# Performance work log

Measured on AMD Instinct MI355X. Metric: run time of the kernel, lower is better.

Reference implementation:

```python
import math
import jax, jax.numpy as jnp
import numpy as np


def setup_inputs() -> dict:
    key = jax.random.key(0)
    k1, k2, k3 = jax.random.split(key, 3)
    mk = jax.random.normal(k1, (4, 64, 8, 32, 32), dtype=jnp.float32)
    qk = jax.random.normal(k2, (4, 64, 32, 32), dtype=jnp.float32)
    mv = jax.random.normal(k3, (4, 512, 8, 32, 32), dtype=jnp.float32)
    return {"mk": mk, "qk": qk, "mv": mv}


def reference(mk, qk, mv):
    B, CK, T, H, W = mk.shape
    CV = mv.shape[1]
    mkf = mk.reshape(B, CK, T * H * W)          # [B, CK, N]  (memory tokens)
    qkf = qk.reshape(B, CK, H * W)              # [B, CK, M]  (query tokens)
    # L2-distance style affinity: (2*a.b - |a|^2) / sqrt(CK)
    a_sq = jnp.sum(mkf * mkf, axis=1)[:, :, None]              # [B, N, 1]
    ab = jnp.einsum('bcn,bcm->bnm', mkf, qkf)                  # [B, N, M]
    affinity = (2.0 * ab - a_sq) / math.sqrt(CK)
    affinity = jax.nn.softmax(affinity, axis=1)                # softmax over memory dim
    # readout: weighted sum of memory values
    mo = mv.reshape(B, CV, T * H * W)                          # [B, CV, N]
    mem = jnp.einsum('bcn,bnm->bcm', mo, affinity)             # [B, CV, M]
    return mem.reshape(B, CV, H, W)
```

## Files before the change

kernel.cpp:

```cpp
#include <hip/hip_runtime.h>


typedef unsigned short ushort_t;
typedef unsigned int uint_t;
typedef __attribute__((ext_vector_type(8))) short short8;
typedef __attribute__((ext_vector_type(4))) float floatx4;

#define MFMA16(a, b, c) __builtin_amdgcn_mfma_f32_16x16x32_bf16((a), (b), (c), 0, 0, 0)

#define BARRIER_DS() do {                                          \
    asm volatile("s_waitcnt lgkmcnt(0)" ::: "memory");             \
    __builtin_amdgcn_s_barrier();                                  \
} while (0)

__device__ __forceinline__ ushort_t f2b(float f) {
    uint_t b = __float_as_uint(f);
    b += 0x7FFFu + ((b >> 16) & 1u);
    return (ushort_t)(b >> 16);
}

__device__ __forceinline__ short8 pack8(floatx4 a, floatx4 b) {
    short8 r;
    r[0] = (short)f2b(a[0]); r[1] = (short)f2b(a[1]);
    r[2] = (short)f2b(a[2]); r[3] = (short)f2b(a[3]);
    r[4] = (short)f2b(b[0]); r[5] = (short)f2b(b[1]);
    r[6] = (short)f2b(b[2]); r[7] = (short)f2b(b[3]);
    return r;
}

#define BB 4
#define CK 64
#define NN 8192
#define MM 1024
#define CV 512
#define NSTEP 128

__device__ __align__(16) ushort_t g_mkT[BB * NN * CK];
__device__ __align__(16) float    g_asq8[BB * NN];

__global__ __launch_bounds__(256) void k_prep(const float* __restrict__ mk) {
    int t = blockIdx.x * 256 + threadIdx.x;
    int b = t >> 13;
    int n = t & (NN - 1);
    const float* src = mk + (size_t)b * CK * NN + n;
    ushort_t* dst = g_mkT + (size_t)t * CK;
    float acc = 0.f;
#pragma unroll
    for (int g = 0; g < 8; g++) {
        float f[8];
#pragma unroll
        for (int i = 0; i < 8; i++) {
            f[i] = src[(size_t)(g * 8 + i) * NN];
            acc += f[i] * f[i];
        }
        uint4 q;
        q.x = (uint_t)f2b(f[0]) | ((uint_t)f2b(f[1]) << 16);
        q.y = (uint_t)f2b(f[2]) | ((uint_t)f2b(f[3]) << 16);
        q.z = (uint_t)f2b(f[4]) | ((uint_t)f2b(f[5]) << 16);
        q.w = (uint_t)f2b(f[6]) | ((uint_t)f2b(f[7]) << 16);
        *(uint4*)(dst + g * 8) = q;
    }
    g_asq8[t] = acc * 0.125f;
}


#define STEP(KC0, KC1, AC, MC0, MC1, MC2, MC3, KN0, KN1, AN, MN0, MN1, MN2, MN3, stepv) do { \
    if ((stepv) + 1 < NSTEP) {                                                  \
        size_t no = (size_t)((stepv) + 1) * 64;                                 \
        const ushort_t* kp = kbase + no * CK;                                   \
        KN0 = *(const short8*)kp;                                               \
        KN1 = *(const short8*)(kp + 32);                                        \
        AN  = asbase[no];                                                       \
        MN0 = *(const floatx4*)(mvbase + no);                                   \
        MN1 = *(const floatx4*)(mvbase + no + 4);                               \
        MN2 = *(const floatx4*)(mvbase + no + 32);                              \
        MN3 = *(const floatx4*)(mvbase + no + 36);                              \
    }                                                                           \
    _Pragma("unroll")                                                           \
    for (int mt = 0; mt < 4; mt++) {                                            \
        floatx4 d = (floatx4){0.f, 0.f, 0.f, 0.f};                              \
        d = MFMA16(qb0[mt], KC0, d);                                            \
        d = MFMA16(qb1[mt], KC1, d);                                            \
        _Pragma("unroll")                                                       \
        for (int r = 0; r < 4; r++) {                                           \
            float p = __expf(d[r] * 0.25f - AC);                                \
            dpart[mt][r] += p;                                                  \
            lds_p[(mt * 16 + quad * 4 + r) * 72 + w * 16 + l15] = f2b(p);       \
        }                                                                       \
    }                                                                           \
    BARRIER_DS();        \
    {                                                                           \
        short8 va0 = pack8(MC0, MC1);                                           \
        short8 va1 = pack8(MC2, MC3);                                           \
        _Pragma("unroll")                                                       \
        for (int mt = 0; mt < 4; mt++) {                                        \
            short8 pb0 = *(const short8*)&lds_p[(mt * 16 + l15) * 72 + quad * 8];        \
            short8 pb1 = *(const short8*)&lds_p[(mt * 16 + l15) * 72 + 32 + quad * 8];   \
            acc[mt] = MFMA16(va0, pb0, acc[mt]);                                \
            acc[mt] = MFMA16(va1, pb1, acc[mt]);                                \
        }                                                                       \
    }                                                                           \
    BARRIER_DS();                         \
} while (0)

__global__ __launch_bounds__(256, 2) void k_main(const float* __restrict__ qk,
                                                 const float* __restrict__ mv,
                                                 float* __restrict__ out) {
    __shared__ __align__(16) ushort_t lds_p[64 * 72];
    __shared__ float dn[64];

    int bx = blockIdx.x;
    int mt16 = bx >> 5;
    int cs = (bx >> 2) & 7;
    int b = bx & 3;
    int c0 = cs * 64;
    int m0 = mt16 * 64;

    int tid = threadIdx.x;
    int w = tid >> 6;
    int lane = tid & 63;
    int quad = lane >> 4;
    int l15 = lane & 15;

    if (tid < 64) dn[tid] = 0.f;

    short8 qb0[4], qb1[4];
#pragma unroll
    for (int mt = 0; mt < 4; mt++) {
#pragma unroll
        for (int j = 0; j < 8; j++) {
            qb0[mt][j] = (short)f2b(qk[(size_t)(b * CK + quad * 8 + j) * MM + m0 + mt * 16 + l15]);
            qb1[mt][j] = (short)f2b(qk[(size_t)(b * CK + 32 + quad * 8 + j) * MM + m0 + mt * 16 + l15]);
        }
    }

    const ushort_t* kbase  = g_mkT + ((size_t)b * NN + w * 16 + l15) * CK + quad * 8;
    const float*    asbase = g_asq8 + (size_t)b * NN + w * 16 + l15;
    const float*    mvbase = mv + ((size_t)(b * CV + c0 + w * 16 + l15)) * NN + quad * 8;

    floatx4 acc[4];
#pragma unroll
    for (int i = 0; i < 4; i++) acc[i] = (floatx4){0.f, 0.f, 0.f, 0.f};
    float dpart[4][4];
#pragma unroll
    for (int i = 0; i < 4; i++)
#pragma unroll
        for (int j = 0; j < 4; j++) dpart[i][j] = 0.f;

    short8 kA0, kA1, kB0, kB1;
    floatx4 mA0, mA1, mA2, mA3, mB0, mB1, mB2, mB3;
    float aA, aB;
    kA0 = *(const short8*)kbase;
    kA1 = *(const short8*)(kbase + 32);
    aA  = *asbase;
    mA0 = *(const floatx4*)(mvbase);
    mA1 = *(const floatx4*)(mvbase + 4);
    mA2 = *(const floatx4*)(mvbase + 32);
    mA3 = *(const floatx4*)(mvbase + 36);

    for (int sp = 0; sp < NSTEP / 2; sp++) {
        STEP(kA0, kA1, aA, mA0, mA1, mA2, mA3, kB0, kB1, aB, mB0, mB1, mB2, mB3, sp * 2);
        STEP(kB0, kB1, aB, mB0, mB1, mB2, mB3, kA0, kA1, aA, mA0, mA1, mA2, mA3, sp * 2 + 1);
    }

#pragma unroll
    for (int mt = 0; mt < 4; mt++) {
#pragma unroll
        for (int r = 0; r < 4; r++) {
            float s = dpart[mt][r];
            s += __shfl_xor(s, 1, 64);
            s += __shfl_xor(s, 2, 64);
            s += __shfl_xor(s, 4, 64);
            s += __shfl_xor(s, 8, 64);
            if (l15 == 0) atomicAdd(&dn[mt * 16 + quad * 4 + r], s);
        }
    }
    __syncthreads();

    float rdm[4];
#pragma unroll
    for (int mt = 0; mt < 4; mt++) rdm[mt] = 1.0f / dn[mt * 16 + l15];
#pragma unroll
    for (int mt = 0; mt < 4; mt++) {
#pragma unroll
        for (int r = 0; r < 4; r++) {
            size_t o = (size_t)(b * CV + c0 + w * 16 + quad * 4 + r) * MM
                     + m0 + mt * 16 + l15;
            out[o] = acc[mt][r] * rdm[mt];
        }
    }
}

extern "C" void kernel_launch(void* const* d_in, const int* in_sizes, int n_in,
                              void* d_out, int out_size, void* d_ws, size_t ws_size,
                              hipStream_t stream) {
    const float* mk = nullptr;
    const float* qk = nullptr;
    const float* mv = nullptr;
    for (int i = 0; i < n_in; i++) {
        if (in_sizes[i] == BB * CK * NN)      mk = (const float*)d_in[i];
        else if (in_sizes[i] == BB * CK * MM) qk = (const float*)d_in[i];
        else if (in_sizes[i] == BB * CV * NN) mv = (const float*)d_in[i];
    }
    float* out = (float*)d_out;
    (void)d_ws; (void)ws_size; (void)out_size;

    k_prep<<<(BB * NN) / 256, 256, 0, stream>>>(mk);
    k_main<<<16 * 8 * BB, 256, 0, stream>>>(qk, mv, out);
}
```

Baseline: 270.4 us.

## Split memory dimension across two blocks with reduction kernel; coalesce prep transpose

Splits the N (memory token) loop into two halves handled by separate blocks, doubling the grid from 512 to 1024 blocks and raising occupancy hints. Partial numerators and denominators go to global scratch and a new reduce kernel combines and normalizes them. The prep kernel is rewritten to transpose mk through LDS with vectorized coalesced loads. The split adds an extra kernel launch, a partial-result round trip through global memory, and reloads qk once per half. The softmax stays correct because the exponentials carry no max subtraction.

```diff
diff --git a/kernel.cpp b/kernel.cpp
--- a/kernel.cpp
+++ b/kernel.cpp
@@ -33,39 +33,59 @@
 #define NN 8192
 #define MM 1024
 #define CV 512
-#define NSTEP 128
+#define NH 2
+#define NSTEP_H 64
 
 __device__ __align__(16) ushort_t g_mkT[BB * NN * CK];
 __device__ __align__(16) float    g_asq8[BB * NN];
+__device__ __align__(16) float    g_pacc[1024 * 64 * 64];
+__device__ __align__(16) float    g_pdn[1024 * 64];
 
 __global__ __launch_bounds__(256) void k_prep(const float* __restrict__ mk) {
-    int t = blockIdx.x * 256 + threadIdx.x;
-    int b = t >> 13;
-    int n = t & (NN - 1);
-    const float* src = mk + (size_t)b * CK * NN + n;
-    ushort_t* dst = g_mkT + (size_t)t * CK;
-    float acc = 0.f;
-#pragma unroll
-    for (int g = 0; g < 8; g++) {
-        float f[8];
-#pragma unroll
-        for (int i = 0; i < 8; i++) {
-            f[i] = src[(size_t)(g * 8 + i) * NN];
-            acc += f[i] * f[i];
-        }
-        uint4 q;
-        q.x = (uint_t)f2b(f[0]) | ((uint_t)f2b(f[1]) << 16);
-        q.y = (uint_t)f2b(f[2]) | ((uint_t)f2b(f[3]) << 16);
-        q.z = (uint_t)f2b(f[4]) | ((uint_t)f2b(f[5]) << 16);
-        q.w = (uint_t)f2b(f[6]) | ((uint_t)f2b(f[7]) << 16);
-        *(uint4*)(dst + g * 8) = q;
-    }
-    g_asq8[t] = acc * 0.125f;
+    __shared__ float lds_t[64][68];
+    int bx = blockIdx.x;
+    int b = bx >> 7;
+    int nt = bx & 127;
+    int tid = threadIdx.x;
+    int cc = tid >> 2, seg = tid & 3;
+    const float* src = mk + ((size_t)(b * CK + cc)) * NN + nt * 64 + seg * 16;
+#pragma unroll
+    for (int g = 0; g < 4; g++) {
+        floatx4 v = *(const floatx4*)(src + g * 4);
+        lds_t[seg * 16 + g * 4 + 0][cc] = v[0];
+        lds_t[seg * 16 + g * 4 + 1][cc] = v[1];
+        lds_t[seg * 16 + g * 4 + 2][cc] = v[2];
+        lds_t[seg * 16 + g * 4 + 3][cc] = v[3];
+    }
+    __syncthreads();
+    int n = tid >> 2;
+    const float* row = &lds_t[n][seg * 16];
+    float v[16];
+#pragma unroll
+    for (int i = 0; i < 16; i++) v[i] = row[i];
+    float sq = 0.f;
+#pragma unroll
+    for (int i = 0; i < 16; i++) sq = fmaf(v[i], v[i], sq);
+    sq += __shfl_xor(sq, 1, 64);
+    sq += __shfl_xor(sq, 2, 64);
+    uint4 q0, q1;
+    q0.x = (uint_t)f2b(v[0])  | ((uint_t)f2b(v[1])  << 16);
+    q0.y = (uint_t)f2b(v[2])  | ((uint_t)f2b(v[3])  << 16);
+    q0.z = (uint_t)f2b(v[4])  | ((uint_t)f2b(v[5])  << 16);
+    q0.w = (uint_t)f2b(v[6])  | ((uint_t)f2b(v[7])  << 16);
+    q1.x = (uint_t)f2b(v[8])  | ((uint_t)f2b(v[9])  << 16);
+    q1.y = (uint_t)f2b(v[10]) | ((uint_t)f2b(v[11]) << 16);
+    q1.z = (uint_t)f2b(v[12]) | ((uint_t)f2b(v[13]) << 16);
+    q1.w = (uint_t)f2b(v[14]) | ((uint_t)f2b(v[15]) << 16);
+    ushort_t* dst = g_mkT + ((size_t)b * NN + nt * 64 + n) * CK + seg * 16;
+    *(uint4*)dst = q0;
+    *(uint4*)(dst + 8) = q1;
+    if (seg == 0) g_asq8[(size_t)b * NN + nt * 64 + n] = sq * 0.125f;
 }
 
 
 #define STEP(KC0, KC1, AC, MC0, MC1, MC2, MC3, KN0, KN1, AN, MN0, MN1, MN2, MN3, stepv) do { \
-    if ((stepv) + 1 < NSTEP) {                                                  \
+    if ((stepv) + 1 < NSTEP_H) {                                                \
         size_t no = (size_t)((stepv) + 1) * 64;                                 \
         const ushort_t* kp = kbase + no * CK;                                   \
         KN0 = *(const short8*)kp;                                               \
@@ -103,18 +123,19 @@
     BARRIER_DS();                         \
 } while (0)
 
-__global__ __launch_bounds__(256, 2) void k_main(const float* __restrict__ qk,
-                                                 const float* __restrict__ mv,
-                                                 float* __restrict__ out) {
+__global__ __launch_bounds__(256, 4) void k_main(const float* __restrict__ qk,
+                                                 const float* __restrict__ mv) {
     __shared__ __align__(16) ushort_t lds_p[64 * 72];
     __shared__ float dn[64];
 
     int bx = blockIdx.x;
-    int mt16 = bx >> 5;
-    int cs = (bx >> 2) & 7;
-    int b = bx & 3;
+    int mt16 = bx >> 6;
+    int cs = (bx >> 3) & 7;
+    int b = (bx >> 1) & 3;
+    int nh = bx & 1;
     int c0 = cs * 64;
     int m0 = mt16 * 64;
+    int n0 = nh * (NN / NH);
 
     int tid = threadIdx.x;
     int w = tid >> 6;
@@ -134,9 +155,9 @@
         }
     }
 
-    const ushort_t* kbase  = g_mkT + ((size_t)b * NN + w * 16 + l15) * CK + quad * 8;
-    const float*    asbase = g_asq8 + (size_t)b * NN + w * 16 + l15;
-    const float*    mvbase = mv + ((size_t)(b * CV + c0 + w * 16 + l15)) * NN + quad * 8;
+    const ushort_t* kbase  = g_mkT + ((size_t)b * NN + n0 + w * 16 + l15) * CK + quad * 8;
+    const float*    asbase = g_asq8 + (size_t)b * NN + n0 + w * 16 + l15;
+    const float*    mvbase = mv + ((size_t)(b * CV + c0 + w * 16 + l15)) * NN + n0 + quad * 8;
 
     floatx4 acc[4];
 #pragma unroll
@@ -158,7 +179,7 @@
     mA2 = *(const floatx4*)(mvbase + 32);
     mA3 = *(const floatx4*)(mvbase + 36);
 
-    for (int sp = 0; sp < NSTEP / 2; sp++) {
+    for (int sp = 0; sp < NSTEP_H / 2; sp++) {
         STEP(kA0, kA1, aA, mA0, mA1, mA2, mA3, kB0, kB1, aB, mB0, mB1, mB2, mB3, sp * 2);
         STEP(kB0, kB1, aB, mB0, mB1, mB2, mB3, kA0, kA1, aA, mA0, mA1, mA2, mA3, sp * 2 + 1);
     }
@@ -177,17 +198,43 @@
     }
     __syncthreads();
 
-    float rdm[4];
-#pragma unroll
-    for (int mt = 0; mt < 4; mt++) rdm[mt] = 1.0f / dn[mt * 16 + l15];
+    float* pa = g_pacc + (size_t)bx * 4096;
 #pragma unroll
     for (int mt = 0; mt < 4; mt++) {
 #pragma unroll
-        for (int r = 0; r < 4; r++) {
-            size_t o = (size_t)(b * CV + c0 + w * 16 + quad * 4 + r) * MM
-                     + m0 + mt * 16 + l15;
-            out[o] = acc[mt][r] * rdm[mt];
-        }
+        for (int r = 0; r < 4; r++)
+            pa[(w * 16 + quad * 4 + r) * 64 + mt * 16 + l15] = acc[mt][r];
+    }
+    if (tid < 64) g_pdn[(size_t)bx * 64 + tid] = dn[tid];
+}
+
+__global__ __launch_bounds__(256) void k_reduce(float* __restrict__ out) {
+    __shared__ float rdm[64];
+    int bxr = blockIdx.x;
+    int mt16 = bxr >> 5;
+    int cs = (bxr >> 2) & 7;
+    int b = bxr & 3;
+    int tid = threadIdx.x;
+
+    const float* p0 = g_pacc + (size_t)(2 * bxr) * 4096;
+    const float* p1 = g_pacc + (size_t)(2 * bxr + 1) * 4096;
+    if (tid < 64)
+        rdm[tid] = 1.0f / (g_pdn[(size_t)(2 * bxr) * 64 + tid] +
+                           g_pdn[(size_t)(2 * bxr + 1) * 64 + tid]);
+    __syncthreads();
+
+    int c_loc = tid >> 2;
+    int mseg = (tid & 3) * 16;
+    size_t pbase = (size_t)c_loc * 64 + mseg;
+    size_t obase = (size_t)(b * CV + cs * 64 + c_loc) * MM + mt16 * 64 + mseg;
+#pragma unroll
+    for (int g4 = 0; g4 < 4; g4++) {
+        floatx4 a = *(const floatx4*)(p0 + pbase + g4 * 4);
+        floatx4 bb = *(const floatx4*)(p1 + pbase + g4 * 4);
+        floatx4 r;
+#pragma unroll
+        for (int j = 0; j < 4; j++) r[j] = (a[j] + bb[j]) * rdm[mseg + g4 * 4 + j];
+        *(floatx4*)(out + obase + g4 * 4) = r;
     }
 }
 
@@ -205,6 +252,7 @@
     float* out = (float*)d_out;
     (void)d_ws; (void)ws_size; (void)out_size;
 
-    k_prep<<<(BB * NN) / 256, 256, 0, stream>>>(mk);
-    k_main<<<16 * 8 * BB, 256, 0, stream>>>(qk, mv, out);
-}
+    k_prep<<<BB * 128, 256, 0, stream>>>(mk);
+    k_main<<<16 * 8 * BB * NH, 256, 0, stream>>>(qk, mv);
+    k_reduce<<<16 * 8 * BB, 256, 0, stream>>>(out);
+}
```

New measurement: 372.7 us. 37.8% more time.

## Split main kernel into producer/consumer waves with double-buffered P tile

Applied to the files above, without the earlier changes.

The main kernel moves to 512 threads. Four producer waves compute the affinity exponentials into one of two LDS buffers while four consumer waves load mv and run the readout MFMAs on the other buffer, so the exp/softmax stage and the value GEMM overlap across steps. The prep kernel now transposes mk through LDS with coalesced vector loads instead of strided scalar reads. The trade-offs are more threads per block, doubled LDS, and producers and consumers staying in lockstep through barriers.

```diff
diff --git a/kernel.cpp b/kernel.cpp
--- a/kernel.cpp
+++ b/kernel.cpp
@@ -39,43 +39,64 @@
 __device__ __align__(16) float    g_asq8[BB * NN];
 
 __global__ __launch_bounds__(256) void k_prep(const float* __restrict__ mk) {
-    int t = blockIdx.x * 256 + threadIdx.x;
-    int b = t >> 13;
-    int n = t & (NN - 1);
-    const float* src = mk + (size_t)b * CK * NN + n;
-    ushort_t* dst = g_mkT + (size_t)t * CK;
-    float acc = 0.f;
-#pragma unroll
-    for (int g = 0; g < 8; g++) {
-        float f[8];
-#pragma unroll
-        for (int i = 0; i < 8; i++) {
-            f[i] = src[(size_t)(g * 8 + i) * NN];
-            acc += f[i] * f[i];
-        }
-        uint4 q;
-        q.x = (uint_t)f2b(f[0]) | ((uint_t)f2b(f[1]) << 16);
-        q.y = (uint_t)f2b(f[2]) | ((uint_t)f2b(f[3]) << 16);
-        q.z = (uint_t)f2b(f[4]) | ((uint_t)f2b(f[5]) << 16);
-        q.w = (uint_t)f2b(f[6]) | ((uint_t)f2b(f[7]) << 16);
-        *(uint4*)(dst + g * 8) = q;
-    }
-    g_asq8[t] = acc * 0.125f;
-}
-
-
-#define STEP(KC0, KC1, AC, MC0, MC1, MC2, MC3, KN0, KN1, AN, MN0, MN1, MN2, MN3, stepv) do { \
-    if ((stepv) + 1 < NSTEP) {                                                  \
-        size_t no = (size_t)((stepv) + 1) * 64;                                 \
-        const ushort_t* kp = kbase + no * CK;                                   \
-        KN0 = *(const short8*)kp;                                               \
-        KN1 = *(const short8*)(kp + 32);                                        \
-        AN  = asbase[no];                                                       \
-        MN0 = *(const floatx4*)(mvbase + no);                                   \
-        MN1 = *(const floatx4*)(mvbase + no + 4);                               \
-        MN2 = *(const floatx4*)(mvbase + no + 32);                              \
-        MN3 = *(const floatx4*)(mvbase + no + 36);                              \
-    }                                                                           \
+    __shared__ float lds_t[64][68];
+    int bx = blockIdx.x;
+    int b = bx >> 7;
+    int nt = bx & 127;
+    int tid = threadIdx.x;
+    int cc = tid >> 2, seg = tid & 3;
+    const float* src = mk + ((size_t)(b * CK + cc)) * NN + nt * 64 + seg * 16;
+#pragma unroll
+    for (int g = 0; g < 4; g++) {
+        floatx4 v = *(const floatx4*)(src + g * 4);
+        lds_t[seg * 16 + g * 4 + 0][cc] = v[0];
+        lds_t[seg * 16 + g * 4 + 1][cc] = v[1];
+        lds_t[seg * 16 + g * 4 + 2][cc] = v[2];
+        lds_t[seg * 16 + g * 4 + 3][cc] = v[3];
+    }
+    __syncthreads();
+    int n = tid >> 2;
+    const float* row = &lds_t[n][seg * 16];
+    float v[16];
+#pragma unroll
+    for (int i = 0; i < 16; i++) v[i] = row[i];
+    float sq = 0.f;
+#pragma unroll
+    for (int i = 0; i < 16; i++) sq = fmaf(v[i], v[i], sq);
+    sq += __shfl_xor(sq, 1, 64);
+    sq += __shfl_xor(sq, 2, 64);
+    uint4 q0, q1;
+    q0.x = (uint_t)f2b(v[0])  | ((uint_t)f2b(v[1])  << 16);
+    q0.y = (uint_t)f2b(v[2])  | ((uint_t)f2b(v[3])  << 16);
+    q0.z = (uint_t)f2b(v[4])  | ((uint_t)f2b(v[5])  << 16);
+    q0.w = (uint_t)f2b(v[6])  | ((uint_t)f2b(v[7])  << 16);
+    q1.x = (uint_t)f2b(v[8])  | ((uint_t)f2b(v[9])  << 16);
+    q1.y = (uint_t)f2b(v[10]) | ((uint_t)f2b(v[11]) << 16);
+    q1.z = (uint_t)f2b(v[12]) | ((uint_t)f2b(v[13]) << 16);
+    q1.w = (uint_t)f2b(v[14]) | ((uint_t)f2b(v[15]) << 16);
+    ushort_t* dst = g_mkT + ((size_t)b * NN + nt * 64 + n) * CK + seg * 16;
+    *(uint4*)dst = q0;
+    *(uint4*)(dst + 8) = q1;
+    if (seg == 0) g_asq8[(size_t)b * NN + nt * 64 + n] = sq * 0.125f;
+}
+
+
+#define PFK(KD0, KD1, AD, sv) do {                                              \
+    const ushort_t* kp = kbase + (size_t)(sv) * 64 * CK;                        \
+    KD0 = *(const short8*)kp;                                                   \
+    KD1 = *(const short8*)(kp + 32);                                            \
+    AD  = asbase[(size_t)(sv) * 64];                                            \
+} while (0)
+
+#define PFM(MD0, MD1, MD2, MD3, sv) do {                                        \
+    const float* mp = mvbase + (size_t)(sv) * 64;                               \
+    MD0 = *(const floatx4*)(mp);                                                \
+    MD1 = *(const floatx4*)(mp + 4);                                            \
+    MD2 = *(const floatx4*)(mp + 32);                                           \
+    MD3 = *(const floatx4*)(mp + 36);                                           \
+} while (0)
+
+#define PSTEP(KC0, KC1, AC, BUFID) do {                                         \
     _Pragma("unroll")                                                           \
     for (int mt = 0; mt < 4; mt++) {                                            \
         floatx4 d = (floatx4){0.f, 0.f, 0.f, 0.f};                              \
@@ -85,28 +106,27 @@
         for (int r = 0; r < 4; r++) {                                           \
             float p = __expf(d[r] * 0.25f - AC);                                \
             dpart[mt][r] += p;                                                  \
-            lds_p[(mt * 16 + quad * 4 + r) * 72 + w * 16 + l15] = f2b(p);       \
+            lds_p[BUFID][(mt * 16 + quad * 4 + r) * 72 + w * 16 + l15] = f2b(p); \
         }                                                                       \
     }                                                                           \
-    BARRIER_DS();        \
-    {                                                                           \
-        short8 va0 = pack8(MC0, MC1);                                           \
-        short8 va1 = pack8(MC2, MC3);                                           \
-        _Pragma("unroll")                                                       \
-        for (int mt = 0; mt < 4; mt++) {                                        \
-            short8 pb0 = *(const short8*)&lds_p[(mt * 16 + l15) * 72 + quad * 8];        \
-            short8 pb1 = *(const short8*)&lds_p[(mt * 16 + l15) * 72 + 32 + quad * 8];   \
-            acc[mt] = MFMA16(va0, pb0, acc[mt]);                                \
-            acc[mt] = MFMA16(va1, pb1, acc[mt]);                                \
-        }                                                                       \
+} while (0)
+
+#define CSTEP(M0, M1, M2, M3, BUFID) do {                                       \
+    short8 va0 = pack8(M0, M1);                                                 \
+    short8 va1 = pack8(M2, M3);                                                 \
+    _Pragma("unroll")                                                           \
+    for (int mt = 0; mt < 4; mt++) {                                            \
+        short8 pb0 = *(const short8*)&lds_p[BUFID][(mt * 16 + l15) * 72 + quad * 8];      \
+        short8 pb1 = *(const short8*)&lds_p[BUFID][(mt * 16 + l15) * 72 + 32 + quad * 8]; \
+        acc[mt] = MFMA16(va0, pb0, acc[mt]);                                    \
+        acc[mt] = MFMA16(va1, pb1, acc[mt]);                                    \
     }                                                                           \
-    BARRIER_DS();                         \
-} while (0)
-
-__global__ __launch_bounds__(256, 2) void k_main(const float* __restrict__ qk,
+} while (0)
+
+__global__ __launch_bounds__(512, 4) void k_main(const float* __restrict__ qk,
                                                  const float* __restrict__ mv,
                                                  float* __restrict__ out) {
-    __shared__ __align__(16) ushort_t lds_p[64 * 72];
+    __shared__ __align__(16) ushort_t lds_p[2][64 * 72];
     __shared__ float dn[64];
 
     int bx = blockIdx.x;
@@ -117,7 +137,9 @@
     int m0 = mt16 * 64;
 
     int tid = threadIdx.x;
-    int w = tid >> 6;
+    int wid = tid >> 6;
+    int w = wid & 3;
+    bool prod = wid < 4;
     int lane = tid & 63;
     int quad = lane >> 4;
     int l15 = lane & 15;
@@ -125,68 +147,84 @@
     if (tid < 64) dn[tid] = 0.f;
 
     short8 qb0[4], qb1[4];
-#pragma unroll
-    for (int mt = 0; mt < 4; mt++) {
-#pragma unroll
-        for (int j = 0; j < 8; j++) {
-            qb0[mt][j] = (short)f2b(qk[(size_t)(b * CK + quad * 8 + j) * MM + m0 + mt * 16 + l15]);
-            qb1[mt][j] = (short)f2b(qk[(size_t)(b * CK + 32 + quad * 8 + j) * MM + m0 + mt * 16 + l15]);
-        }
-    }
+    short8 kA0, kA1, kB0, kB1;
+    float aA, aB;
+    float dpart[4][4];
+    floatx4 mA0, mA1, mA2, mA3, mB0, mB1, mB2, mB3;
+    floatx4 acc[4];
 
     const ushort_t* kbase  = g_mkT + ((size_t)b * NN + w * 16 + l15) * CK + quad * 8;
     const float*    asbase = g_asq8 + (size_t)b * NN + w * 16 + l15;
     const float*    mvbase = mv + ((size_t)(b * CV + c0 + w * 16 + l15)) * NN + quad * 8;
 
-    floatx4 acc[4];
-#pragma unroll
-    for (int i = 0; i < 4; i++) acc[i] = (floatx4){0.f, 0.f, 0.f, 0.f};
-    float dpart[4][4];
-#pragma unroll
-    for (int i = 0; i < 4; i++)
-#pragma unroll
-        for (int j = 0; j < 4; j++) dpart[i][j] = 0.f;
-
-    short8 kA0, kA1, kB0, kB1;
-    floatx4 mA0, mA1, mA2, mA3, mB0, mB1, mB2, mB3;
-    float aA, aB;
-    kA0 = *(const short8*)kbase;
-    kA1 = *(const short8*)(kbase + 32);
-    aA  = *asbase;
-    mA0 = *(const floatx4*)(mvbase);
-    mA1 = *(const floatx4*)(mvbase + 4);
-    mA2 = *(const floatx4*)(mvbase + 32);
-    mA3 = *(const floatx4*)(mvbase + 36);
+    if (prod) {
+#pragma unroll
+        for (int mt = 0; mt < 4; mt++) {
+#pragma unroll
+            for (int j = 0; j < 8; j++) {
+                qb0[mt][j] = (short)f2b(qk[(size_t)(b * CK + quad * 8 + j) * MM + m0 + mt * 16 + l15]);
+                qb1[mt][j] = (short)f2b(qk[(size_t)(b * CK + 32 + quad * 8 + j) * MM + m0 + mt * 16 + l15]);
+            }
+        }
+#pragma unroll
+        for (int i = 0; i < 4; i++)
+#pragma unroll
+            for (int j = 0; j < 4; j++) dpart[i][j] = 0.f;
+        PFK(kA0, kA1, aA, 0);
+    } else {
+#pragma unroll
+        for (int i = 0; i < 4; i++) acc[i] = (floatx4){0.f, 0.f, 0.f, 0.f};
+    }
 
     for (int sp = 0; sp < NSTEP / 2; sp++) {
-        STEP(kA0, kA1, aA, mA0, mA1, mA2, mA3, kB0, kB1, aB, mB0, mB1, mB2, mB3, sp * 2);
-        STEP(kB0, kB1, aB, mB0, mB1, mB2, mB3, kA0, kA1, aA, mA0, mA1, mA2, mA3, sp * 2 + 1);
-    }
-
-#pragma unroll
-    for (int mt = 0; mt < 4; mt++) {
-#pragma unroll
-        for (int r = 0; r < 4; r++) {
-            float s = dpart[mt][r];
-            s += __shfl_xor(s, 1, 64);
-            s += __shfl_xor(s, 2, 64);
-            s += __shfl_xor(s, 4, 64);
-            s += __shfl_xor(s, 8, 64);
-            if (l15 == 0) atomicAdd(&dn[mt * 16 + quad * 4 + r], s);
-        }
+        if (prod) {
+            PFK(kB0, kB1, aB, sp * 2 + 1);
+            PSTEP(kA0, kA1, aA, 0);
+        } else {
+            PFM(mA0, mA1, mA2, mA3, sp * 2);
+            if (sp > 0) CSTEP(mB0, mB1, mB2, mB3, 1);
+        }
+        BARRIER_DS();
+        if (prod) {
+            if (sp + 1 < NSTEP / 2) PFK(kA0, kA1, aA, sp * 2 + 2);
+            PSTEP(kB0, kB1, aB, 1);
+        } else {
+            PFM(mB0, mB1, mB2, mB3, sp * 2 + 1);
+            CSTEP(mA0, mA1, mA2, mA3, 0);
+        }
+        BARRIER_DS();
+    }
+
+    if (prod) {
+#pragma unroll
+        for (int mt = 0; mt < 4; mt++) {
+#pragma unroll
+            for (int r = 0; r < 4; r++) {
+                float s = dpart[mt][r];
+                s += __shfl_xor(s, 1, 64);
+                s += __shfl_xor(s, 2, 64);
+                s += __shfl_xor(s, 4, 64);
+                s += __shfl_xor(s, 8, 64);
+                if (l15 == 0) atomicAdd(&dn[mt * 16 + quad * 4 + r], s);
+            }
+        }
+    } else {
+        CSTEP(mB0, mB1, mB2, mB3, 1);
     }
     __syncthreads();
 
-    float rdm[4];
-#pragma unroll
-    for (int mt = 0; mt < 4; mt++) rdm[mt] = 1.0f / dn[mt * 16 + l15];
-#pragma unroll
-    for (int mt = 0; mt < 4; mt++) {
-#pragma unroll
-        for (int r = 0; r < 4; r++) {
-            size_t o = (size_t)(b * CV + c0 + w * 16 + quad * 4 + r) * MM
-                     + m0 + mt * 16 + l15;
-            out[o] = acc[mt][r] * rdm[mt];
+    if (!prod) {
+        float rdm[4];
+#pragma unroll
+        for (int mt = 0; mt < 4; mt++) rdm[mt] = 1.0f / dn[mt * 16 + l15];
+#pragma unroll
+        for (int mt = 0; mt < 4; mt++) {
+#pragma unroll
+            for (int r = 0; r < 4; r++) {
+                size_t o = (size_t)(b * CV + c0 + w * 16 + quad * 4 + r) * MM
+                         + m0 + mt * 16 + l15;
+                out[o] = acc[mt][r] * rdm[mt];
+            }
         }
     }
 }
@@ -205,6 +243,6 @@
     float* out = (float*)d_out;
     (void)d_ws; (void)ws_size; (void)out_size;
 
-    k_prep<<<(BB * NN) / 256, 256, 0, stream>>>(mk);
-    k_main<<<16 * 8 * BB, 256, 0, stream>>>(qk, mv, out);
-}
+    k_prep<<<BB * 128, 256, 0, stream>>>(mk);
+    k_main<<<16 * 8 * BB, 512, 0, stream>>>(qk, mv, out);
+}
```

Result: slower. 380.5 us (+40.7%).

## Fuse key prep into main kernel, loading fp32 keys and computing norms inline

Applied to the files above, without the earlier changes.

Removes the separate prep kernel that transposed mk to bf16 and precomputed squared norms. The main kernel now reads fp32 keys directly with strided column loads, computes the per-token squared norm with cross-lane shuffles, and converts to bf16 in registers each step. This drops a kernel launch and the intermediate global round-trip. In exchange, each of the 8 channel-slice blocks per batch reloads and reconverts the keys, and each step issues 16 scalar strided loads, which adds redundant traffic and register pressure.

```diff
diff --git a/kernel.cpp b/kernel.cpp
--- a/kernel.cpp
+++ b/kernel.cpp
@@ -35,52 +35,42 @@
 #define CV 512
 #define NSTEP 128
 
-__device__ __align__(16) ushort_t g_mkT[BB * NN * CK];
-__device__ __align__(16) float    g_asq8[BB * NN];
 
-__global__ __launch_bounds__(256) void k_prep(const float* __restrict__ mk) {
-    int t = blockIdx.x * 256 + threadIdx.x;
-    int b = t >> 13;
-    int n = t & (NN - 1);
-    const float* src = mk + (size_t)b * CK * NN + n;
-    ushort_t* dst = g_mkT + (size_t)t * CK;
-    float acc = 0.f;
-#pragma unroll
-    for (int g = 0; g < 8; g++) {
-        float f[8];
-#pragma unroll
-        for (int i = 0; i < 8; i++) {
-            f[i] = src[(size_t)(g * 8 + i) * NN];
-            acc += f[i] * f[i];
-        }
-        uint4 q;
-        q.x = (uint_t)f2b(f[0]) | ((uint_t)f2b(f[1]) << 16);
-        q.y = (uint_t)f2b(f[2]) | ((uint_t)f2b(f[3]) << 16);
-        q.z = (uint_t)f2b(f[4]) | ((uint_t)f2b(f[5]) << 16);
-        q.w = (uint_t)f2b(f[6]) | ((uint_t)f2b(f[7]) << 16);
-        *(uint4*)(dst + g * 8) = q;
-    }
-    g_asq8[t] = acc * 0.125f;
-}
+#define PF(FN, MN0, MN1, MN2, MN3, sv) do {                                     \
+    size_t no = (size_t)(sv) * 64;                                              \
+    _Pragma("unroll")                                                           \
+    for (int j = 0; j < 8; j++) {                                               \
+        FN[j]     = kb[(size_t)j * NN + no];                                    \
+        FN[j + 8] = kb[(size_t)(32 + j) * NN + no];                             \
+    }                                                                           \
+    const float* mp = mvbase + no;                                              \
+    MN0 = *(const floatx4*)(mp);                                                \
+    MN1 = *(const floatx4*)(mp + 4);                                            \
+    MN2 = *(const floatx4*)(mp + 32);                                           \
+    MN3 = *(const floatx4*)(mp + 36);                                           \
+} while (0)
 
-
-#define STEP(KC0, KC1, AC, MC0, MC1, MC2, MC3, KN0, KN1, AN, MN0, MN1, MN2, MN3, stepv) do { \
-    if ((stepv) + 1 < NSTEP) {                                                  \
-        size_t no = (size_t)((stepv) + 1) * 64;                                 \
-        const ushort_t* kp = kbase + no * CK;                                   \
-        KN0 = *(const short8*)kp;                                               \
-        KN1 = *(const short8*)(kp + 32);                                        \
-        AN  = asbase[no];                                                       \
-        MN0 = *(const floatx4*)(mvbase + no);                                   \
-        MN1 = *(const floatx4*)(mvbase + no + 4);                               \
-        MN2 = *(const floatx4*)(mvbase + no + 32);                              \
-        MN3 = *(const floatx4*)(mvbase + no + 36);                              \
+#define STEPX(FC, MC0, MC1, MC2, MC3, FN, MN0, MN1, MN2, MN3, stepv) do {       \
+    if ((stepv) + 1 < NSTEP) { PF(FN, MN0, MN1, MN2, MN3, (stepv) + 1); }       \
+                             \
+    float sq = 0.f;                                                             \
+    _Pragma("unroll")                                                           \
+    for (int i = 0; i < 16; i++) sq = fmaf(FC[i], FC[i], sq);                   \
+    sq += __shfl_xor(sq, 16, 64);                                               \
+    sq += __shfl_xor(sq, 32, 64);                                               \
+    float AC = sq * 0.125f;                                                     \
+    short8 kc0, kc1;                                                            \
+    _Pragma("unroll")                                                           \
+    for (int j = 0; j < 8; j++) {                                               \
+        kc0[j] = (short)f2b(FC[j]);                                             \
+        kc1[j] = (short)f2b(FC[j + 8]);                                         \
     }                                                                           \
+              \
     _Pragma("unroll")                                                           \
     for (int mt = 0; mt < 4; mt++) {                                            \
         floatx4 d = (floatx4){0.f, 0.f, 0.f, 0.f};                              \
-        d = MFMA16(qb0[mt], KC0, d);                                            \
-        d = MFMA16(qb1[mt], KC1, d);                                            \
+        d = MFMA16(qb0[mt], kc0, d);                                            \
+        d = MFMA16(qb1[mt], kc1, d);                                            \
         _Pragma("unroll")                                                       \
         for (int r = 0; r < 4; r++) {                                           \
             float p = __expf(d[r] * 0.25f - AC);                                \
@@ -104,6 +94,7 @@
 } while (0)
 
 __global__ __launch_bounds__(256, 2) void k_main(const float* __restrict__ qk,
+                                                 const float* __restrict__ mk,
                                                  const float* __restrict__ mv,
                                                  float* __restrict__ out) {
     __shared__ __align__(16) ushort_t lds_p[64 * 72];
@@ -134,9 +125,8 @@
         }
     }
 
-    const ushort_t* kbase  = g_mkT + ((size_t)b * NN + w * 16 + l15) * CK + quad * 8;
-    const float*    asbase = g_asq8 + (size_t)b * NN + w * 16 + l15;
-    const float*    mvbase = mv + ((size_t)(b * CV + c0 + w * 16 + l15)) * NN + quad * 8;
+    const float* kb     = mk + ((size_t)(b * CK) + quad * 8) * NN + w * 16 + l15;
+    const float* mvbase = mv + ((size_t)(b * CV + c0 + w * 16 + l15)) * NN + quad * 8;
 
     floatx4 acc[4];
 #pragma unroll
@@ -147,20 +137,13 @@
 #pragma unroll
         for (int j = 0; j < 4; j++) dpart[i][j] = 0.f;
 
-    short8 kA0, kA1, kB0, kB1;
+    float fA[16], fB[16];
     floatx4 mA0, mA1, mA2, mA3, mB0, mB1, mB2, mB3;
-    float aA, aB;
-    kA0 = *(const short8*)kbase;
-    kA1 = *(const short8*)(kbase + 32);
-    aA  = *asbase;
-    mA0 = *(const floatx4*)(mvbase);
-    mA1 = *(const floatx4*)(mvbase + 4);
-    mA2 = *(const floatx4*)(mvbase + 32);
-    mA3 = *(const floatx4*)(mvbase + 36);
+    PF(fA, mA0, mA1, mA2, mA3, 0);
 
     for (int sp = 0; sp < NSTEP / 2; sp++) {
-        STEP(kA0, kA1, aA, mA0, mA1, mA2, mA3, kB0, kB1, aB, mB0, mB1, mB2, mB3, sp * 2);
-        STEP(kB0, kB1, aB, mB0, mB1, mB2, mB3, kA0, kA1, aA, mA0, mA1, mA2, mA3, sp * 2 + 1);
+        STEPX(fA, mA0, mA1, mA2, mA3, fB, mB0, mB1, mB2, mB3, sp * 2);
+        STEPX(fB, mB0, mB1, mB2, mB3, fA, mA0, mA1, mA2, mA3, sp * 2 + 1);
     }
 
 #pragma unroll
@@ -205,6 +188,5 @@
     float* out = (float*)d_out;
     (void)d_ws; (void)ws_size; (void)out_size;
 
-    k_prep<<<(BB * NN) / 256, 256, 0, stream>>>(mk);
-    k_main<<<16 * 8 * BB, 256, 0, stream>>>(qk, mv, out);
+    k_main<<<16 * 8 * BB, 256, 0, stream>>>(qk, mk, mv, out);
 }
```

New measurement: 295.8 us. 9.4% more time.
